# Kernel optimization log

Hardware: AMD Instinct MI355X
Metric: run time of the kernel (lower is better)

## Reference

```python
import jax, jax.numpy as jnp
import numpy as np

BATCH, N_FREQ, N_TIME = 32, 128, 8192


def setup_inputs() -> dict:
    key = jax.random.key(0)
    spectrogram = jax.random.normal(key, (BATCH, N_FREQ, N_TIME), dtype=jnp.float32)
    return {"spectrogram": spectrogram, "source_pt": 4000, "dest_pt": 4050}


def _time_warp(spectrogram, source_pt, dest_pt):
    # spectrogram: [B, n_freq, n_time]
    _, n_freq, n_time = spectrogram.shape
    left_ratio = dest_pt / source_pt
    right_ratio = (n_time - dest_pt) / (n_time - source_pt)

    t = jnp.arange(n_time, dtype=jnp.float32)
    indices = jnp.where(t < dest_pt, t / left_ratio,
                        source_pt + (t - dest_pt) / right_ratio)
    indices = jnp.clip(indices, 0.0, n_time - 1)  # [n_time]

    # Faithful to source: grid channel 0 (grid_sample's x) = grid_y values,
    # channel 1 (grid_sample's y) = warped time values -> axes swapped.
    # align_corners=True: pix = (coord + 1)/2 * (size - 1)
    x_pix = jnp.arange(n_freq, dtype=jnp.float32) / (n_freq - 1) * (n_time - 1)  # [n_freq]
    y_pix = indices / (n_time - 1) * (n_freq - 1)                                # [n_time]

    # padding_mode='border': clamp sample coords into valid range
    x_pix = jnp.clip(x_pix, 0.0, n_time - 1)
    y_pix = jnp.clip(y_pix, 0.0, n_freq - 1)

    x0 = jnp.floor(x_pix).astype(jnp.int32)
    x1 = jnp.minimum(x0 + 1, n_time - 1)
    y0 = jnp.floor(y_pix).astype(jnp.int32)
    y1 = jnp.minimum(y0 + 1, n_freq - 1)
    wx = (x_pix - x0.astype(jnp.float32))[:, None]   # [n_freq, 1] (output freq axis)
    wy = (y_pix - y0.astype(jnp.float32))[None, :]   # [1, n_time] (output time axis)

    def gather(yi, xi):
        # out[b, i, j] = spectrogram[b, yi[j], xi[i]]
        return spectrogram[:, yi[None, :], xi[:, None]]  # [B, n_freq, n_time]

    out = ((1.0 - wy) * (1.0 - wx)) * gather(y0, x0) \
        + ((1.0 - wy) * wx) * gather(y0, x1) \
        + (wy * (1.0 - wx)) * gather(y1, x0) \
        + (wy * wx) * gather(y1, x1)
    return out


def reference(spectrogram, source_pt, dest_pt):
    return _time_warp(spectrogram, source_pt, dest_pt)
```

## Files before the change

### kernel.cpp

```cpp
#include <hip/hip_runtime.h>

#define BATCH 32
#define NFREQ 128
#define NTIME 8192
#define NROWS (BATCH * NFREQ)

__global__ __launch_bounds__(256) void gather_blend_kernel(
    const float* __restrict__ S,
    float* __restrict__ W)
{
    const int tid = blockIdx.x * 256 + threadIdx.x;
    const int i   = tid & (NFREQ - 1);
    const int ry  = tid >> 7;

    const float Tm1 = (float)(NTIME - 1);
    const float Fm1 = (float)(NFREQ - 1);

    float x_pix = ((float)i / Fm1) * Tm1;
    x_pix = fminf(fmaxf(x_pix, 0.0f), Tm1);
    const int   x0 = (int)floorf(x_pix);
    const int   x1 = min(x0 + 1, NTIME - 1);
    const float wx = x_pix - (float)x0;

    const float* p = S + (size_t)ry * NTIME;
    const float v0 = p[x0];
    const float v1 = p[x1];
    W[tid] = v0 + wx * (v1 - v0);
}

__global__ __launch_bounds__(256) void stream_kernel(
    const float* __restrict__ W,
    const int* __restrict__ src_p,
    const int* __restrict__ dst_p,
    float* __restrict__ out)
{
    const float sourcef = (float)src_p[0];
    const float destf   = (float)dst_p[0];
    const float Tm1 = (float)(NTIME - 1);
    const float Fm1 = (float)(NFREQ - 1);
    const float inv_left  = sourcef / destf;
    const float inv_right = ((float)NTIME - sourcef) / ((float)NTIME - destf);
    const float y_scale   = Fm1 / Tm1;

    const int row = blockIdx.x;
    const int i   = row & (NFREQ - 1);
    const int b   = row >> 7;

    __shared__ float m[NFREQ];
    if (threadIdx.x < NFREQ) {
        m[threadIdx.x] = W[((size_t)((b << 7) + threadIdx.x) << 7) + i];
    }
    __syncthreads();

    float* orow = out + (size_t)row * NTIME;

#pragma unroll
    for (int c = 0; c < 8; ++c) {
        const int f = c * 256 + threadIdx.x;
        const int j0 = f * 4;
        float4 r;
        float* rp = &r.x;
#pragma unroll
        for (int k = 0; k < 4; ++k) {
            const float t = (float)(j0 + k);
            float idx = (t < destf) ? (t * inv_left)
                                    : fmaf(t - destf, inv_right, sourcef);
            idx = fminf(fmaxf(idx, 0.0f), Tm1);
            float y_pix = idx * y_scale;
            y_pix = fminf(fmaxf(y_pix, 0.0f), Fm1);
            const float y0f = floorf(y_pix);
            const int   y0  = (int)y0f;
            const int   y1  = min(y0 + 1, NFREQ - 1);
            const float wy  = y_pix - y0f;
            const float m0  = m[y0];
            rp[k] = m0 + wy * (m[y1] - m0);
        }
        ((float4*)orow)[f] = r;
    }
}

__global__ __launch_bounds__(256) void timewarp_fused_kernel(
    const float* __restrict__ S,
    const int* __restrict__ src_p,
    const int* __restrict__ dst_p,
    float* __restrict__ out)
{
    const float sourcef = (float)src_p[0];
    const float destf   = (float)dst_p[0];
    const float Tm1 = (float)(NTIME - 1);
    const float Fm1 = (float)(NFREQ - 1);
    const float inv_left  = sourcef / destf;
    const float inv_right = ((float)NTIME - sourcef) / ((float)NTIME - destf);
    const float y_scale   = Fm1 / Tm1;

    const int row = blockIdx.x;
    const int i   = row & (NFREQ - 1);
    const int b   = row >> 7;

    float x_pix = ((float)i / Fm1) * Tm1;
    x_pix = fminf(fmaxf(x_pix, 0.0f), Tm1);
    const int   x0 = (int)floorf(x_pix);
    const int   x1 = min(x0 + 1, NTIME - 1);
    const float wx = x_pix - (float)x0;

    const float* Sb = S + (size_t)b * (NFREQ * NTIME);

    __shared__ float m[NFREQ];
    if (threadIdx.x < NFREQ) {
        const int y = threadIdx.x;
        const float v0 = Sb[(size_t)y * NTIME + x0];
        const float v1 = Sb[(size_t)y * NTIME + x1];
        m[y] = v0 + wx * (v1 - v0);
    }
    __syncthreads();

    float* orow = out + (size_t)row * NTIME;
#pragma unroll
    for (int c = 0; c < 8; ++c) {
        const int f = c * 256 + threadIdx.x;
        const int j0 = f * 4;
        float4 r;
        float* rp = &r.x;
#pragma unroll
        for (int k = 0; k < 4; ++k) {
            const float t = (float)(j0 + k);
            float idx = (t < destf) ? (t * inv_left)
                                    : fmaf(t - destf, inv_right, sourcef);
            idx = fminf(fmaxf(idx, 0.0f), Tm1);
            float y_pix = idx * y_scale;
            y_pix = fminf(fmaxf(y_pix, 0.0f), Fm1);
            const float y0f = floorf(y_pix);
            const int   y0  = (int)y0f;
            const int   y1  = min(y0 + 1, NFREQ - 1);
            const float wy  = y_pix - y0f;
            const float m0  = m[y0];
            rp[k] = m0 + wy * (m[y1] - m0);
        }
        ((float4*)orow)[f] = r;
    }
}

extern "C" void kernel_launch(void* const* d_in, const int* in_sizes, int n_in,
                              void* d_out, int out_size, void* d_ws, size_t ws_size,
                              hipStream_t stream) {
    const float* S   = (const float*)d_in[0];
    const int*   sp  = (const int*)d_in[1];
    const int*   dp  = (const int*)d_in[2];
    float*       out = (float*)d_out;

    const size_t w_bytes = (size_t)NROWS * NFREQ * sizeof(float);

    if (ws_size >= w_bytes) {
        float* W = (float*)d_ws;
        gather_blend_kernel<<<dim3(NROWS * NFREQ / 256), dim3(256), 0, stream>>>(S, W);
        stream_kernel<<<dim3(NROWS), dim3(256), 0, stream>>>(W, sp, dp, out);
    } else {
        timewarp_fused_kernel<<<dim3(NROWS), dim3(256), 0, stream>>>(S, sp, dp, out);
    }
}
```

Measured before the change: 221.9 us.

## Use single fused kernel and split column gathers across all threads

Drops the two-kernel path that staged blended columns in a workspace and always launches the fused kernel. Inside it, the two gathers per frequency row are split across both halves of the block and combined through shared memory. This removes one launch and the workspace round trip. In exchange every block repeats strided gathers from the input and adds an extra barrier.

```diff
diff --git a/kernel.cpp b/kernel.cpp
--- a/kernel.cpp
+++ b/kernel.cpp
@@ -4,80 +4,6 @@
 #define NFREQ 128
 #define NTIME 8192
 #define NROWS (BATCH * NFREQ)
-
-__global__ __launch_bounds__(256) void gather_blend_kernel(
-    const float* __restrict__ S,
-    float* __restrict__ W)
-{
-    const int tid = blockIdx.x * 256 + threadIdx.x;
-    const int i   = tid & (NFREQ - 1);
-    const int ry  = tid >> 7;
-
-    const float Tm1 = (float)(NTIME - 1);
-    const float Fm1 = (float)(NFREQ - 1);
-
-    float x_pix = ((float)i / Fm1) * Tm1;
-    x_pix = fminf(fmaxf(x_pix, 0.0f), Tm1);
-    const int   x0 = (int)floorf(x_pix);
-    const int   x1 = min(x0 + 1, NTIME - 1);
-    const float wx = x_pix - (float)x0;
-
-    const float* p = S + (size_t)ry * NTIME;
-    const float v0 = p[x0];
-    const float v1 = p[x1];
-    W[tid] = v0 + wx * (v1 - v0);
-}
-
-__global__ __launch_bounds__(256) void stream_kernel(
-    const float* __restrict__ W,
-    const int* __restrict__ src_p,
-    const int* __restrict__ dst_p,
-    float* __restrict__ out)
-{
-    const float sourcef = (float)src_p[0];
-    const float destf   = (float)dst_p[0];
-    const float Tm1 = (float)(NTIME - 1);
-    const float Fm1 = (float)(NFREQ - 1);
-    const float inv_left  = sourcef / destf;
-    const float inv_right = ((float)NTIME - sourcef) / ((float)NTIME - destf);
-    const float y_scale   = Fm1 / Tm1;
-
-    const int row = blockIdx.x;
-    const int i   = row & (NFREQ - 1);
-    const int b   = row >> 7;
-
-    __shared__ float m[NFREQ];
-    if (threadIdx.x < NFREQ) {
-        m[threadIdx.x] = W[((size_t)((b << 7) + threadIdx.x) << 7) + i];
-    }
-    __syncthreads();
-
-    float* orow = out + (size_t)row * NTIME;
-
-#pragma unroll
-    for (int c = 0; c < 8; ++c) {
-        const int f = c * 256 + threadIdx.x;
-        const int j0 = f * 4;
-        float4 r;
-        float* rp = &r.x;
-#pragma unroll
-        for (int k = 0; k < 4; ++k) {
-            const float t = (float)(j0 + k);
-            float idx = (t < destf) ? (t * inv_left)
-                                    : fmaf(t - destf, inv_right, sourcef);
-            idx = fminf(fmaxf(idx, 0.0f), Tm1);
-            float y_pix = idx * y_scale;
-            y_pix = fminf(fmaxf(y_pix, 0.0f), Fm1);
-            const float y0f = floorf(y_pix);
-            const int   y0  = (int)y0f;
-            const int   y1  = min(y0 + 1, NFREQ - 1);
-            const float wy  = y_pix - y0f;
-            const float m0  = m[y0];
-            rp[k] = m0 + wy * (m[y1] - m0);
-        }
-        ((float4*)orow)[f] = r;
-    }
-}
 
 __global__ __launch_bounds__(256) void timewarp_fused_kernel(
     const float* __restrict__ S,
@@ -105,16 +31,25 @@
 
     const float* Sb = S + (size_t)b * (NFREQ * NTIME);
 
+    __shared__ float v0s[NFREQ];
+    __shared__ float v1s[NFREQ];
     __shared__ float m[NFREQ];
-    if (threadIdx.x < NFREQ) {
-        const int y = threadIdx.x;
-        const float v0 = Sb[(size_t)y * NTIME + x0];
-        const float v1 = Sb[(size_t)y * NTIME + x1];
-        m[y] = v0 + wx * (v1 - v0);
+
+    const int t = threadIdx.x;
+    if (t < NFREQ) {
+        v0s[t] = Sb[(size_t)t * NTIME + x0];
+    } else {
+        v1s[t - NFREQ] = Sb[(size_t)(t - NFREQ) * NTIME + x1];
+    }
+    __syncthreads();
+    if (t < NFREQ) {
+        const float v0 = v0s[t];
+        m[t] = v0 + wx * (v1s[t] - v0);
     }
     __syncthreads();
 
     float* orow = out + (size_t)row * NTIME;
+
 #pragma unroll
     for (int c = 0; c < 8; ++c) {
         const int f = c * 256 + threadIdx.x;
@@ -123,9 +58,9 @@
         float* rp = &r.x;
 #pragma unroll
         for (int k = 0; k < 4; ++k) {
-            const float t = (float)(j0 + k);
-            float idx = (t < destf) ? (t * inv_left)
-                                    : fmaf(t - destf, inv_right, sourcef);
+            const float t2 = (float)(j0 + k);
+            float idx = (t2 < destf) ? (t2 * inv_left)
+                                     : fmaf(t2 - destf, inv_right, sourcef);
             idx = fminf(fmaxf(idx, 0.0f), Tm1);
             float y_pix = idx * y_scale;
             y_pix = fminf(fmaxf(y_pix, 0.0f), Fm1);
@@ -148,13 +83,7 @@
     const int*   dp  = (const int*)d_in[2];
     float*       out = (float*)d_out;
 
-    const size_t w_bytes = (size_t)NROWS * NFREQ * sizeof(float);
+    (void)d_ws; (void)ws_size;
 
-    if (ws_size >= w_bytes) {
-        float* W = (float*)d_ws;
-        gather_blend_kernel<<<dim3(NROWS * NFREQ / 256), dim3(256), 0, stream>>>(S, W);
-        stream_kernel<<<dim3(NROWS), dim3(256), 0, stream>>>(W, sp, dp, out);
-    } else {
-        timewarp_fused_kernel<<<dim3(NROWS), dim3(256), 0, stream>>>(S, sp, dp, out);
-    }
+    timewarp_fused_kernel<<<dim3(NROWS), dim3(256), 0, stream>>>(S, sp, dp, out);
 }
```

After: 225.6 us. About the same (+1.7%).
